# Kernel optimization log

Measured on AMD Instinct MI355X. Metric: run time of the kernel, lower is better.

Reference implementation:

```python
import jax, jax.numpy as jnp
import numpy as np

# dims
B, S, T, F = 8, 1024, 32, 64       # batch, stocks(nodes), seq_len, feature
DWV = 64                            # d_word_vec == d_model
RNN = 64                            # GRU hidden (rnn_unit)
NHID = 128                          # n_hid
NH, DK, DV = 4, 16, 16              # heads, d_k, d_v
NC, NE = 2, 128                     # n_class, num hyperedges (H.shape[1])


def setup_inputs() -> dict:
    key = jax.random.key(0)
    ks = jax.random.split(key, 24)
    def p(i, shape):
        return jax.random.normal(ks[i], shape, jnp.float32) / np.float32(np.sqrt(shape[-1]))
    return {
        'src_seq': jax.random.normal(ks[0], (B, S, T, F), jnp.float32),
        'H': jax.random.normal(ks[1], (S, NE), jnp.float32) * 0.1,
        'adj': jax.random.normal(ks[2], (S, S), jnp.float32) * 0.02,
        'n_hid': NHID,
        # GCN (feature -> n_hid -> feature), shared across both adj and H_new branches
        'gcn_W1': p(3, (F, NHID)), 'gcn_b1': jnp.zeros((NHID,), jnp.float32),
        'gcn_W2': p(4, (NHID, F)), 'gcn_b2': jnp.zeros((F,), jnp.float32),
        # Linear(H.shape[1] -> H.shape[0]) created inside forward
        'Wm': p(5, (S, NE)) * 0.1, 'bm': jnp.zeros((S,), jnp.float32),
        # Linear(feature -> d_word_vec)
        'Wl': p(6, (DWV, F)), 'bl': jnp.zeros((DWV,), jnp.float32),
        # 2-layer GRU (batch_first), torch layout W_{ir|iz|in} stacked
        'Wx0': p(7, (3 * RNN, DWV)), 'Wh0': p(8, (3 * RNN, RNN)),
        'bx0': jnp.zeros((3 * RNN,), jnp.float32), 'bh0': jnp.zeros((3 * RNN,), jnp.float32),
        'Wx1': p(9, (3 * RNN, RNN)), 'Wh1': p(10, (3 * RNN, RNN)),
        'bx1': jnp.zeros((3 * RNN,), jnp.float32), 'bh1': jnp.zeros((3 * RNN,), jnp.float32),
        # temporal multi-head attention
        'Wq': p(11, (NH * DK, RNN)), 'Wk': p(12, (NH * DK, RNN)), 'Wv': p(13, (NH * DV, RNN)),
        'Wo': p(14, (RNN, NH * DV)),
        'ln_g': jnp.ones((RNN,), jnp.float32), 'ln_b': jnp.zeros((RNN,), jnp.float32),
        # HGN: two graph-conv layers over stocks, (T*RNN -> n_hid -> n_hid)
        'Wg1': p(15, (T * RNN, NHID)), 'Wg2': p(16, (NHID, NHID)),
        # tgt_word_prj: n_hid -> n_class (no bias)
        'Wp': p(17, (NC, NHID)),
    }


def reference(src_seq, H, adj, n_hid, gcn_W1, gcn_b1, gcn_W2, gcn_b2, Wm, bm,
              Wl, bl, Wx0, Wh0, bx0, bh0, Wx1, Wh1, bx1, bh1,
              Wq, Wk, Wv, Wo, ln_g, ln_b, Wg1, Wg2, Wp):
    b, s, t, f = src_seq.shape

    # per-timestep GCN over the stock (node) axis, fully batched (replaces the
    # double Python loop of mm+spmm in the original)
    def gcn(x, A):  # x: (b,s,t,f), A: (s,s)
        h = jax.nn.relu(jnp.einsum('nm,bmth->bnth', A, x @ gcn_W1) + gcn_b1)
        return jnp.einsum('nm,bmtf->bntf', A, h @ gcn_W2) + gcn_b2

    H_new = H @ Wm.T + bm                       # (s,s) learned hypergraph adjacency
    z = gcn(src_seq, adj) + gcn(src_seq, H_new)  # y_i + y_f for all timesteps

    x = (z @ Wl.T + bl).reshape(b * s, t, -1)    # (N, T, DWV)
    n = b * s

    def gru_layer(xin, Wx, Wh, bx, bh):
        hdim = Wh.shape[1]
        xp = xin @ Wx.T + bx                      # precompute input projections (N,T,3H)
        def step(h, xt):
            gh = h @ Wh.T + bh
            xr, xz, xn = jnp.split(xt, 3, -1)
            hr, hz, hn = jnp.split(gh, 3, -1)
            r = jax.nn.sigmoid(xr + hr)
            zg = jax.nn.sigmoid(xz + hz)
            cand = jnp.tanh(xn + r * hn)
            hnew = (1.0 - zg) * cand + zg * h
            return hnew, hnew
        h0 = jnp.zeros((xin.shape[0], hdim), xin.dtype)
        _, ys = jax.lax.scan(step, h0, jnp.swapaxes(xp, 0, 1))
        return jnp.swapaxes(ys, 0, 1)

    r = gru_layer(gru_layer(x, Wx0, Wh0, bx0, bh0), Wx1, Wh1, bx1, bh1)  # (N,T,RNN)

    # temporal multi-head self-attention with causal (subsequent) mask
    q = (r @ Wq.T).reshape(n, t, NH, DK)
    k = (r @ Wk.T).reshape(n, t, NH, DK)
    v = (r @ Wv.T).reshape(n, t, NH, DV)
    scores = jnp.einsum('nqhd,nkhd->nhqk', q, k) / np.float32(np.sqrt(DK))
    causal = jnp.triu(jnp.ones((t, t), bool), 1)
    attn = jax.nn.softmax(jnp.where(causal, jnp.float32(-1e9), scores), -1)
    o = jnp.einsum('nhqk,nkhd->nqhd', attn, v).reshape(n, t, NH * DV) @ Wo.T + r
    mu = o.mean(-1, keepdims=True)
    o = (o - mu) / jnp.sqrt(o.var(-1, keepdims=True) + 1e-6) * ln_g + ln_b

    enc = o.reshape(b, s, t * o.shape[-1])        # (b, s, T*RNN)

    # HGN: two graph convolutions over the stock axis -> (b, s, n_hid)
    hg = jax.nn.relu(jnp.einsum('nm,bmd->bnd', adj, enc @ Wg1))
    hg = jnp.einsum('nm,bmd->bnd', adj, hg @ Wg2)

    return hg.reshape(b * s, -1) @ Wp.T           # x_logit_scale = 1.0 (no weight sharing)
```

## Files before the change

kernel.cpp:

```cpp
#include <hip/hip_runtime.h>

typedef __attribute__((ext_vector_type(8))) short bf8;
typedef __attribute__((ext_vector_type(4))) float f4;

__device__ __forceinline__ ushort f2b(float f) {
  union { float f; unsigned u; } v; v.f = f;
  unsigned u = v.u + 0x7FFFu + ((v.u >> 16) & 1u);
  return (ushort)(u >> 16);
}
__device__ __forceinline__ float b2f(ushort h) {
  union { unsigned u; float f; } v; v.u = ((unsigned)h) << 16; return v.f;
}
__device__ __forceinline__ bf8 pack8(const float* p) {
  f4 a = *(const f4*)p; f4 b = *(const f4*)(p + 4);
  bf8 t;
  t[0] = (short)f2b(a[0]); t[1] = (short)f2b(a[1]);
  t[2] = (short)f2b(a[2]); t[3] = (short)f2b(a[3]);
  t[4] = (short)f2b(b[0]); t[5] = (short)f2b(b[1]);
  t[6] = (short)f2b(b[2]); t[7] = (short)f2b(b[3]);
  return t;
}
__device__ __forceinline__ float sigm(float x) { return 1.f / (1.f + __expf(-x)); }
__device__ __forceinline__ float tanh_f(float x) {
  float a = fabsf(x), e = __expf(-2.f * a);
  return copysignf((1.f - e) / (1.f + e), x);
}

__device__ __forceinline__ void gl16(const void* g, void* l) {
  __builtin_amdgcn_global_load_lds(
      (const __attribute__((address_space(1))) unsigned int*)(uintptr_t)g,
      (__attribute__((address_space(3))) unsigned int*)(uintptr_t)l, 16, 0, 0);
}

#define SFENCE __builtin_amdgcn_sched_barrier(0)
#define RAWBAR { __builtin_amdgcn_s_barrier(); SFENCE; }
#define WAIT_LGKM0 { asm volatile("s_waitcnt lgkmcnt(0)" ::: "memory"); SFENCE; }
#define WAIT_VM(n) { asm volatile("s_waitcnt vmcnt(" #n ")" ::: "memory"); SFENCE; }

__global__ __launch_bounds__(256) void cvt_k(const float* __restrict__ in,
                                             ushort* __restrict__ out, int n4) {
  int i = blockIdx.x * 256 + threadIdx.x;
  if (i < n4) {
    f4 v = ((const f4*)in)[i];
    ushort4 o;
    o.x = f2b(v[0]); o.y = f2b(v[1]); o.z = f2b(v[2]); o.w = f2b(v[3]);
    ((ushort4*)out)[i] = o;
  }
}

__global__ __launch_bounds__(256) void cvtT_k(const float* __restrict__ in,
                                              ushort* __restrict__ out, int R, int C) {
  __shared__ ushort t[64][68];
  const int tid = threadIdx.x;
  const int r0 = blockIdx.x * 64, c0 = blockIdx.y * 64;
  #pragma unroll
  for (int it = 0; it < 4; ++it) {
    int r = (tid >> 4) + 16 * it, c = (tid & 15) * 4;
    f4 v = *(const f4*)(in + (long)(r0 + r) * C + c0 + c);
    #pragma unroll
    for (int j = 0; j < 4; ++j) t[c + j][r] = f2b(v[j]);
  }
  __syncthreads();
  #pragma unroll
  for (int it = 0; it < 4; ++it) {
    int cc = (tid >> 4) + 16 * it, rr = (tid & 15) * 4;
    ushort4 o = { t[cc][rr], t[cc][rr + 1], t[cc][rr + 2], t[cc][rr + 3] };
    *(ushort4*)(out + (long)(c0 + cc) * R + r0 + rr) = o;
  }
}

__global__ __launch_bounds__(256) void cat_k(const ushort* __restrict__ a,
                                             const ushort* __restrict__ h,
                                             ushort* __restrict__ o) {
  int i = blockIdx.x * 256 + threadIdx.x;
  int s = i >> 7, c8 = (i & 127) << 3;
  *(int4*)(o + (long)s * 2048 + c8) = *(const int4*)(a + (long)s * 1024 + c8);
  *(int4*)(o + (long)s * 2048 + 1024 + c8) = *(const int4*)(h + (long)s * 1024 + c8);
}

__global__ void wcombT_k(const float* __restrict__ Wl, const float* __restrict__ W2,
                         ushort* __restrict__ out) {
  int idx = blockIdx.x * 256 + threadIdx.x;
  int d = idx >> 7, h = idx & 127;
  float s = 0.f;
  #pragma unroll
  for (int f = 0; f < 64; ++f) s += Wl[d * 64 + f] * W2[h * 64 + f];
  out[d * 128 + h] = f2b(s);
}
__global__ void biasc_k(const float* __restrict__ gb2, const float* __restrict__ Wl,
                        const float* __restrict__ bl, float* __restrict__ bc) {
  int d = threadIdx.x;
  float s = 0.f;
  #pragma unroll
  for (int f = 0; f < 64; ++f) s += gb2[f] * Wl[d * 64 + f];
  bc[d] = 2.f * s + bl[d];
}
__global__ void wfin_k(const float* __restrict__ Wg2, const float* __restrict__ Wp,
                       float* __restrict__ wf) {
  int idx = threadIdx.x;
  int d = idx >> 1, c = idx & 1;
  float s = 0.f;
  #pragma unroll
  for (int e = 0; e < 128; ++e) s += Wg2[d * 128 + e] * Wp[c * 128 + e];
  wf[idx] = s;
}

template<int BIASMODE, int RELU, int OUTMODE>
__global__ __launch_bounds__(512, 2) void gemm3_k(
    const ushort* __restrict__ A, const ushort* __restrict__ B,
    ushort* __restrict__ C, const float* __restrict__ bias, int biasMask,
    int N, int K, int lda, int ldb, int ldc,
    long sAq, long sBq, long sCq)
{
  __shared__ __align__(16) ushort As[2 * 256 * 64];
  __shared__ __align__(16) ushort Bs[2 * 256 * 64];
  const int tid = threadIdx.x, lane = tid & 63, wv = tid >> 6;
  const int wm = wv >> 2, wn = wv & 3;
  const long bm = (long)blockIdx.x * 256, bn = (long)blockIdx.y * 256;
  const int z = blockIdx.z;
  const ushort* Ap = A + (long)z * sAq + bm * lda;
  const ushort* Bp = B + (long)z * sBq + bn * ldb;
  ushort* Cp = C + (long)z * sCq;
  const int nt = K >> 6;

  const int srow = wv * 32 + (lane >> 3);
  const int scol = ((lane & 7) ^ (srow & 7)) << 3;
  const ushort* apb = Ap + (long)srow * lda + scol;
  const ushort* bpb = Bp + (long)srow * ldb + scol;

  #define STAGE3(T, D) { \
    const ushort* ap_ = apb + (T) * 64; \
    const ushort* bp_ = bpb + (T) * 64; \
    ushort* la_ = &As[(D) * 16384 + (wv * 32) * 64]; \
    ushort* lb_ = &Bs[(D) * 16384 + (wv * 32) * 64]; \
    _Pragma("unroll") \
    for (int i_ = 0; i_ < 4; ++i_) gl16(ap_ + (long)(i_ * 8) * lda, la_ + i_ * 512); \
    _Pragma("unroll") \
    for (int i_ = 0; i_ < 4; ++i_) gl16(bp_ + (long)(i_ * 8) * ldb, lb_ + i_ * 512); \
  }

  STAGE3(0, 0);
  if (nt > 1) { STAGE3(1, 1); WAIT_VM(8); }
  else        { WAIT_VM(0); }
  RAWBAR;

  f4 acc[8][4] = {};
  for (int t = 0; t < nt; ++t) {
    const int d = t & 1;
    const ushort* as = As + d * 16384;
    const ushort* bs = Bs + d * 16384;
    bf8 b0[4], a0[8];
    #pragma unroll
    for (int n = 0; n < 4; ++n) {
      int r = wn * 64 + n * 16 + (lane & 15);
      b0[n] = *(const bf8*)(bs + r * 64 + (((lane >> 4) ^ (r & 7)) << 3));
    }
    #pragma unroll
    for (int m = 0; m < 8; ++m) {
      int r = wm * 128 + m * 16 + (lane & 15);
      a0[m] = *(const bf8*)(as + r * 64 + (((lane >> 4) ^ (r & 7)) << 3));
    }
    __builtin_amdgcn_s_setprio(1);
    #pragma unroll
    for (int m = 0; m < 8; ++m)
      #pragma unroll
      for (int n = 0; n < 4; ++n)
        acc[m][n] = __builtin_amdgcn_mfma_f32_16x16x32_bf16(a0[m], b0[n], acc[m][n], 0, 0, 0);
    __builtin_amdgcn_s_setprio(0);
    bf8 b1[4], a1[8];
    #pragma unroll
    for (int n = 0; n < 4; ++n) {
      int r = wn * 64 + n * 16 + (lane & 15);
      b1[n] = *(const bf8*)(bs + r * 64 + (((4 + (lane >> 4)) ^ (r & 7)) << 3));
    }
    #pragma unroll
    for (int m = 0; m < 8; ++m) {
      int r = wm * 128 + m * 16 + (lane & 15);
      a1[m] = *(const bf8*)(as + r * 64 + (((4 + (lane >> 4)) ^ (r & 7)) << 3));
    }
    WAIT_LGKM0;
    RAWBAR;
    if (t + 2 < nt) STAGE3(t + 2, d);
    __builtin_amdgcn_s_setprio(1);
    #pragma unroll
    for (int m = 0; m < 8; ++m)
      #pragma unroll
      for (int n = 0; n < 4; ++n)
        acc[m][n] = __builtin_amdgcn_mfma_f32_16x16x32_bf16(a1[m], b1[n], acc[m][n], 0, 0, 0);
    __builtin_amdgcn_s_setprio(0);
    if (t + 1 < nt) {
      if (t + 2 < nt) { WAIT_VM(8); }
      else            { WAIT_VM(0); }
      RAWBAR;
    }
  }
  #undef STAGE3

  #pragma unroll
  for (int m = 0; m < 8; ++m) {
    int grow = (int)bm + wm * 128 + m * 16 + ((lane >> 4) << 2);
    #pragma unroll
    for (int n = 0; n < 4; ++n) {
      int col = (int)bn + wn * 64 + n * 16 + (lane & 15);
      if (OUTMODE == 2) {
        int hh = grow & 127, tt = grow >> 7;
        ushort4 o;
        o.x = f2b(acc[m][n][0]); o.y = f2b(acc[m][n][1]);
        o.z = f2b(acc[m][n][2]); o.w = f2b(acc[m][n][3]);
        *(ushort4*)(Cp + ((long)col * 32 + tt) * 128 + hh) = o;
      } else {
        #pragma unroll
        for (int rr = 0; rr < 4; ++rr) {
          float v = acc[m][n][rr];
          if (BIASMODE == 1) v += bias[col & biasMask];
          if (BIASMODE == 2) v += bias[(grow + rr) & biasMask];
          if (RELU) v = fmaxf(v, 0.f);
          Cp[(long)(grow + rr) * ldc + col] = f2b(v);
        }
      }
    }
  }
}

template<int BIASMODE, int RELU, int OUTMODE, int SWZ>
__global__ __launch_bounds__(256) void gemm2_k(
    const ushort* __restrict__ A, const ushort* __restrict__ B,
    ushort* __restrict__ C, const float* __restrict__ bias, int biasMask,
    int N, int K, int lda, int ldb, int ldc, int ZD,
    long sAq, long sAr, long sBq, long sBr, long sCq, long sCr)
{
  __shared__ __align__(16) ushort As[2 * 128 * 64];
  __shared__ __align__(16) ushort Bs[2 * 128 * 64];
  const int tid = threadIdx.x, lane = tid & 63, wv = tid >> 6;
  const int wm = wv >> 1, wn = wv & 1;
  int bx = blockIdx.x, by = blockIdx.y;
  if (SWZ) {
    int f = bx + by * gridDim.x;
    int q = f >> 3;
    by = q % gridDim.y;
    bx = (f & 7) + 8 * (q / gridDim.y);
  }
  const long bm = (long)bx * 128, bn = (long)by * 128;
  int z = blockIdx.z, zq = z, zr = 0;
  if (ZD > 1) { zq = z / ZD; zr = z - zq * ZD; }
  const ushort* Ap = A + (long)zq * sAq + (long)zr * sAr + bm * lda;
  const ushort* Bp = B + (long)zq * sBq + (long)zr * sBr + bn * ldb;
  ushort* Cp = C + (long)zq * sCq + (long)zr * sCr;
  const int nt = K >> 6;

  const int srow = wv * 32 + (lane >> 3);
  const int scol = ((lane & 7) ^ (srow & 7)) << 3;
  const ushort* apb = Ap + (long)srow * lda + scol;
  const ushort* bpb = Bp + (long)srow * ldb + scol;

  #define STAGE(T, D) { \
    const ushort* ap_ = apb + (T) * 64; \
    const ushort* bp_ = bpb + (T) * 64; \
    ushort* la_ = &As[((D) * 128 + wv * 32) * 64]; \
    ushort* lb_ = &Bs[((D) * 128 + wv * 32) * 64]; \
    _Pragma("unroll") \
    for (int i_ = 0; i_ < 4; ++i_) gl16(ap_ + (long)(i_ * 8) * lda, la_ + i_ * 512); \
    _Pragma("unroll") \
    for (int i_ = 0; i_ < 4; ++i_) gl16(bp_ + (long)(i_ * 8) * ldb, lb_ + i_ * 512); \
  }

  STAGE(0, 0);
  if (nt > 1) { STAGE(1, 1); WAIT_VM(8); }
  else        { WAIT_VM(0); }
  RAWBAR;

  f4 acc[4][4] = {};
  for (int t = 0; t < nt; ++t) {
    const int d = t & 1;
    const ushort* as = As + d * 8192;
    const ushort* bs = Bs + d * 8192;
    bf8 af[4][2], bfv[4][2];
    #pragma unroll
    for (int mi = 0; mi < 4; ++mi) {
      int r = wm * 64 + mi * 16 + (lane & 15);
      #pragma unroll
      for (int kk = 0; kk < 2; ++kk) {
        int blk = kk * 4 + (lane >> 4);
        af[mi][kk] = *(const bf8*)(as + r * 64 + ((blk ^ (r & 7)) << 3));
      }
    }
    #pragma unroll
    for (int ni = 0; ni < 4; ++ni) {
      int r = wn * 64 + ni * 16 + (lane & 15);
      #pragma unroll
      for (int kk = 0; kk < 2; ++kk) {
        int blk = kk * 4 + (lane >> 4);
        bfv[ni][kk] = *(const bf8*)(bs + r * 64 + ((blk ^ (r & 7)) << 3));
      }
    }
    WAIT_LGKM0;
    RAWBAR;
    if (t + 2 < nt) STAGE(t + 2, d);
    #pragma unroll
    for (int kk = 0; kk < 2; ++kk)
      #pragma unroll
      for (int mi = 0; mi < 4; ++mi)
        #pragma unroll
        for (int ni = 0; ni < 4; ++ni)
          acc[mi][ni] = __builtin_amdgcn_mfma_f32_16x16x32_bf16(af[mi][kk], bfv[ni][kk], acc[mi][ni], 0, 0, 0);
    if (t + 1 < nt) {
      if (t + 2 < nt) { WAIT_VM(8); }
      else            { WAIT_VM(0); }
      RAWBAR;
    }
  }
  #undef STAGE

  #pragma unroll
  for (int mi = 0; mi < 4; ++mi)
    #pragma unroll
    for (int ni = 0; ni < 4; ++ni) {
      int col = (int)bn + wn * 64 + ni * 16 + (lane & 15);
      if (col < N) {
        if (OUTMODE == 2) {
          int hh = wm * 64 + mi * 16 + (lane >> 4) * 4;
          int tt = (int)(bm >> 7);
          ushort4 o;
          o.x = f2b(acc[mi][ni][0]); o.y = f2b(acc[mi][ni][1]);
          o.z = f2b(acc[mi][ni][2]); o.w = f2b(acc[mi][ni][3]);
          *(ushort4*)(Cp + ((long)col * 32 + tt) * 128 + hh) = o;
        } else {
          #pragma unroll
          for (int rr = 0; rr < 4; ++rr) {
            int row = (int)bm + wm * 64 + mi * 16 + (lane >> 4) * 4 + rr;
            float v = acc[mi][ni][rr];
            if (BIASMODE == 1) v += bias[col & biasMask];
            if (BIASMODE == 2) v += bias[row & biasMask];
            if (RELU) v = fmaxf(v, 0.f);
            Cp[(long)row * ldc + col] = f2b(v);
          }
        }
      }
    }
}

template<int BIASMODE, int RELU, int FULLB, int OUTMODE, int SWZ>
__global__ __launch_bounds__(256) void gemm_k(
    const ushort* __restrict__ A, const ushort* __restrict__ B,
    ushort* __restrict__ C, const float* __restrict__ bias, int biasMask,
    int N, int K, int lda, int ldb, int ldc, int ZD,
    long sAq, long sAr, long sBq, long sBr, long sCq, long sCr)
{
  __shared__ __align__(16) ushort As[128 * 64];
  __shared__ __align__(16) ushort Bs[128 * 64];
  const int tid = threadIdx.x, lane = tid & 63, wv = tid >> 6;
  const int wm = wv >> 1, wn = wv & 1;
  int bx = blockIdx.x, by = blockIdx.y;
  const long bm = (long)bx * 128, bn = (long)by * 128;
  int z = blockIdx.z, zq = z, zr = 0;
  if (ZD > 1) { zq = z / ZD; zr = z - zq * ZD; }
  const ushort* Ap = A + (long)zq * sAq + (long)zr * sAr + bm * lda;
  const ushort* Bp = B + (long)zq * sBq + (long)zr * sBr + bn * ldb;
  ushort* Cp = C + (long)zq * sCq + (long)zr * sCr;
  f4 acc[4][4] = {};
  for (int k0 = 0; k0 < K; k0 += 64) {
    #pragma unroll
    for (int i = 0; i < 4; ++i) {
      int row = wv * 32 + i * 8 + (lane >> 3);
      int gc = k0 + (((lane & 7) ^ (row & 7)) << 3);
      gl16(Ap + (long)row * lda + gc, &As[(wv * 32 + i * 8) * 64]);
    }
    if (FULLB) {
      #pragma unroll
      for (int i = 0; i < 4; ++i) {
        int row = wv * 32 + i * 8 + (lane >> 3);
        int gc = k0 + (((lane & 7) ^ (row & 7)) << 3);
        gl16(Bp + (long)row * ldb + gc, &Bs[(wv * 32 + i * 8) * 64]);
      }
    } else {
      #pragma unroll
      for (int i = 0; i < 4; ++i) {
        int row = (tid >> 3) + 32 * i;
        int b8 = tid & 7;
        int4 v = {0, 0, 0, 0};
        if (bn + row < N) v = *(const int4*)(Bp + (long)row * ldb + k0 + ((b8 ^ (row & 7)) << 3));
        *(int4*)(&Bs[row * 64 + b8 * 8]) = v;
      }
    }
    __syncthreads();
    bf8 af[4][2], bfv[4][2];
    #pragma unroll
    for (int mi = 0; mi < 4; ++mi) {
      int r = wm * 64 + mi * 16 + (lane & 15);
      #pragma unroll
      for (int kk = 0; kk < 2; ++kk) {
        int blk = kk * 4 + (lane >> 4);
        af[mi][kk] = *(const bf8*)(&As[r * 64 + ((blk ^ (r & 7)) << 3)]);
      }
    }
    #pragma unroll
    for (int ni = 0; ni < 4; ++ni) {
      int r = wn * 64 + ni * 16 + (lane & 15);
      #pragma unroll
      for (int kk = 0; kk < 2; ++kk) {
        int blk = kk * 4 + (lane >> 4);
        bfv[ni][kk] = *(const bf8*)(&Bs[r * 64 + ((blk ^ (r & 7)) << 3)]);
      }
    }
    #pragma unroll
    for (int kk = 0; kk < 2; ++kk)
      #pragma unroll
      for (int mi = 0; mi < 4; ++mi)
        #pragma unroll
        for (int ni = 0; ni < 4; ++ni)
          acc[mi][ni] = __builtin_amdgcn_mfma_f32_16x16x32_bf16(af[mi][kk], bfv[ni][kk], acc[mi][ni], 0, 0, 0);
    __syncthreads();
  }
  #pragma unroll
  for (int mi = 0; mi < 4; ++mi)
    #pragma unroll
    for (int ni = 0; ni < 4; ++ni) {
      int col = (int)bn + wn * 64 + ni * 16 + (lane & 15);
      if (col < N) {
        #pragma unroll
        for (int rr = 0; rr < 4; ++rr) {
          int row = (int)bm + wm * 64 + mi * 16 + (lane >> 4) * 4 + rr;
          float v = acc[mi][ni][rr];
          if (BIASMODE == 1) v += bias[col & biasMask];
          if (BIASMODE == 2) v += bias[row & biasMask];
          if (RELU) v = fmaxf(v, 0.f);
          long oidx;
          if (OUTMODE == 1) oidx = ((long)(row & 31) * 8192 + (row >> 5)) * 64 + col;
          else              oidx = (long)row * ldc + col;
          Cp[oidx] = f2b(v);
        }
      }
    }
}

__global__ __launch_bounds__(256, 2) void gru_k(
    const ushort* __restrict__ xT,
    const float* __restrict__ Wx0, const float* __restrict__ Wh0,
    const float* __restrict__ bx0, const float* __restrict__ bh0,
    const float* __restrict__ Wx1, const float* __restrict__ Wh1,
    const float* __restrict__ bx1, const float* __restrict__ bh1,
    ushort* __restrict__ rout)
{
  __shared__ ushort hbf[2][2][1024];
  const int tid = threadIdx.x, lane = tid & 63, w = tid >> 6;
  const int seq0 = blockIdx.x * 16;
  for (int i = tid; i < 4096; i += 256) ((ushort*)hbf)[i] = 0;

  const float* Wxp[2] = {Wx0, Wx1};
  const float* Whp[2] = {Wh0, Wh1};
  const float* bxp[2] = {bx0, bx1};
  const float* bhp[2] = {bh0, bh1};
  bf8 Wxf[2][3][2], Whf[2][3][2];
  float bxv[2][3], bhv[2][3];
  #pragma unroll
  for (int L = 0; L < 2; ++L)
    #pragma unroll
    for (int g = 0; g < 3; ++g) {
      int row = g * 64 + w * 16 + (lane & 15);
      bxv[L][g] = bxp[L][row];
      bhv[L][g] = bhp[L][row];
      #pragma unroll
      for (int kk = 0; kk < 2; ++kk) {
        int kb = kk * 32 + (lane >> 4) * 8;
        Wxf[L][g][kk] = pack8(Wxp[L] + row * 64 + kb);
        Whf[L][g][kk] = pack8(Whp[L] + row * 64 + kb);
      }
    }
  __syncthreads();

  const int arow = lane & 15;
  const int col = w * 16 + (lane & 15);
  f4 hprev[2] = {{0.f,0.f,0.f,0.f},{0.f,0.f,0.f,0.f}};
  int pv = 0;
  for (int t = 0; t < 32; ++t) {
    const int cur = pv ^ 1;
    #pragma unroll
    for (int L = 0; L < 2; ++L) {
      bf8 axf[2], ahf[2];
      if (L == 0) {
        const ushort* xb = xT + ((long)t * 8192 + seq0 + arow) * 64 + (lane >> 4) * 8;
        axf[0] = *(const bf8*)(xb);
        axf[1] = *(const bf8*)(xb + 32);
      } else {
        #pragma unroll
        for (int kk = 0; kk < 2; ++kk) {
          int blk = kk * 4 + (lane >> 4);
          axf[kk] = *(const bf8*)(&hbf[0][cur][arow * 64 + ((blk ^ (arow & 7)) << 3)]);
        }
      }
      #pragma unroll
      for (int kk = 0; kk < 2; ++kk) {
        int blk = kk * 4 + (lane >> 4);
        ahf[kk] = *(const bf8*)(&hbf[L][pv][arow * 64 + ((blk ^ (arow & 7)) << 3)]);
      }
      f4 aX[3] = {}; f4 aH[3] = {};
      #pragma unroll
      for (int kk = 0; kk < 2; ++kk)
        #pragma unroll
        for (int g = 0; g < 3; ++g) {
          aX[g] = __builtin_amdgcn_mfma_f32_16x16x32_bf16(axf[kk], Wxf[L][g][kk], aX[g], 0, 0, 0);
          aH[g] = __builtin_amdgcn_mfma_f32_16x16x32_bf16(ahf[kk], Whf[L][g][kk], aH[g], 0, 0, 0);
        }
      f4 hn;
      #pragma unroll
      for (int r = 0; r < 4; ++r) {
        float rg = sigm(aX[0][r] + bxv[L][0] + aH[0][r] + bhv[L][0]);
        float zg = sigm(aX[1][r] + bxv[L][1] + aH[1][r] + bhv[L][1]);
        float cand = tanh_f(aX[2][r] + bxv[L][2] + rg * (aH[2][r] + bhv[L][2]));
        hn[r] = (1.f - zg) * cand + zg * hprev[L][r];
      }
      hprev[L] = hn;
      #pragma unroll
      for (int r = 0; r < 4; ++r) {
        int row = (lane >> 4) * 4 + r;
        ushort hb = f2b(hn[r]);
        hbf[L][cur][row * 64 + (((col >> 3) ^ (row & 7)) << 3) + (col & 7)] = hb;
        if (L == 1) rout[((long)(seq0 + row) * 32 + t) * 64 + col] = hb;
      }
      __syncthreads();
    }
    pv = cur;
  }
}

__global__ __launch_bounds__(256) void attn_k(
    const ushort* __restrict__ r,
    const float* __restrict__ Wq, const float* __restrict__ Wk,
    const float* __restrict__ Wv, const float* __restrict__ Wo,
    const float* __restrict__ lng, const float* __restrict__ lnb,
    ushort* __restrict__ enc)
{
  __shared__ ushort q_s[4][32][40];
  __shared__ ushort k_s[4][32][40];
  __shared__ ushort v_s[4][16][40];
  __shared__ ushort p_s[4][32][40];
  __shared__ ushort o_s[32][88];
  __shared__ float  ln_s[32][68];
  const int tid = threadIdx.x, lane = tid & 63, w = tid >> 6;
  const long n = blockIdx.x;

  for (int i = tid; i < 4 * 32 * 40; i += 256) { ((ushort*)q_s)[i] = 0; ((ushort*)k_s)[i] = 0; }

  bf8 wqf[2], wkf[2], wvf[2], wof[2];
  #pragma unroll
  for (int kk = 0; kk < 2; ++kk) {
    int row = w * 16 + (lane & 15);
    int kb = kk * 32 + (lane >> 4) * 8;
    wqf[kk] = pack8(Wq + row * 64 + kb);
    wkf[kk] = pack8(Wk + row * 64 + kb);
    wvf[kk] = pack8(Wv + row * 64 + kb);
    wof[kk] = pack8(Wo + row * 64 + kb);
  }
  __syncthreads();

  bf8 ar[2][2];
  #pragma unroll
  for (int mi = 0; mi < 2; ++mi)
    #pragma unroll
    for (int kk = 0; kk < 2; ++kk)
      ar[mi][kk] = *(const bf8*)(r + (n * 32 + mi * 16 + (lane & 15)) * 64 + kk * 32 + (lane >> 4) * 8);
  f4 aq[2] = {}, ak[2] = {}, av[2] = {};
  #pragma unroll
  for (int kk = 0; kk < 2; ++kk)
    #pragma unroll
    for (int mi = 0; mi < 2; ++mi) {
      aq[mi] = __builtin_amdgcn_mfma_f32_16x16x32_bf16(ar[mi][kk], wqf[kk], aq[mi], 0, 0, 0);
      ak[mi] = __builtin_amdgcn_mfma_f32_16x16x32_bf16(ar[mi][kk], wkf[kk], ak[mi], 0, 0, 0);
      av[mi] = __builtin_amdgcn_mfma_f32_16x16x32_bf16(ar[mi][kk], wvf[kk], av[mi], 0, 0, 0);
    }
  #pragma unroll
  for (int mi = 0; mi < 2; ++mi)
    #pragma unroll
    for (int rr = 0; rr < 4; ++rr) {
      int row = mi * 16 + (lane >> 4) * 4 + rr;
      q_s[w][row][lane & 15] = f2b(aq[mi][rr]);
      k_s[w][row][lane & 15] = f2b(ak[mi][rr]);
      v_s[w][lane & 15][row] = f2b(av[mi][rr]);
    }

  bf8 a_q[2], b_k[2];
  #pragma unroll
  for (int mt = 0; mt < 2; ++mt)
    a_q[mt] = *(const bf8*)(&q_s[w][mt * 16 + (lane & 15)][(lane >> 4) * 8]);
  #pragma unroll
  for (int nt = 0; nt < 2; ++nt)
    b_k[nt] = *(const bf8*)(&k_s[w][nt * 16 + (lane & 15)][(lane >> 4) * 8]);
  f4 s_[2][2] = {};
  #pragma unroll
  for (int mt = 0; mt < 2; ++mt)
    #pragma unroll
    for (int nt = 0; nt < 2; ++nt)
      s_[mt][nt] = __builtin_amdgcn_mfma_f32_16x16x32_bf16(a_q[mt], b_k[nt], s_[mt][nt], 0, 0, 0);
  #pragma unroll
  for (int mt = 0; mt < 2; ++mt)
    #pragma unroll
    for (int rr = 0; rr < 4; ++rr) {
      int trow = mt * 16 + (lane >> 4) * 4 + rr;
      float s0 = s_[mt][0][rr] * 0.25f, s1 = s_[mt][1][rr] * 0.25f;
      int c0 = lane & 15, c1 = 16 + (lane & 15);
      if (c0 > trow) s0 = -1e30f;
      if (c1 > trow) s1 = -1e30f;
      float m = fmaxf(s0, s1);
      #pragma unroll
      for (int d = 1; d < 16; d <<= 1) m = fmaxf(m, __shfl_xor(m, d));
      float e0 = __expf(s0 - m), e1 = __expf(s1 - m);
      float sum = e0 + e1;
      #pragma unroll
      for (int d = 1; d < 16; d <<= 1) sum += __shfl_xor(sum, d);
      float inv = 1.f / sum;
      p_s[w][trow][c0] = f2b(e0 * inv);
      p_s[w][trow][c1] = f2b(e1 * inv);
    }

  bf8 b_v = *(const bf8*)(&v_s[w][lane & 15][(lane >> 4) * 8]);
  f4 o_[2] = {};
  #pragma unroll
  for (int mt = 0; mt < 2; ++mt) {
    bf8 a_p = *(const bf8*)(&p_s[w][mt * 16 + (lane & 15)][(lane >> 4) * 8]);
    o_[mt] = __builtin_amdgcn_mfma_f32_16x16x32_bf16(a_p, b_v, o_[mt], 0, 0, 0);
  }
  #pragma unroll
  for (int mt = 0; mt < 2; ++mt)
    #pragma unroll
    for (int rr = 0; rr < 4; ++rr)
      o_s[mt * 16 + (lane >> 4) * 4 + rr][w * 16 + (lane & 15)] = f2b(o_[mt][rr]);
  __syncthreads();

  bf8 a_o[2][2];
  #pragma unroll
  for (int mt = 0; mt < 2; ++mt)
    #pragma unroll
    for (int kk = 0; kk < 2; ++kk)
      a_o[mt][kk] = *(const bf8*)(&o_s[mt * 16 + (lane & 15)][kk * 32 + (lane >> 4) * 8]);
  f4 oo[2] = {};
  #pragma unroll
  for (int kk = 0; kk < 2; ++kk)
    #pragma unroll
    for (int mt = 0; mt < 2; ++mt)
      oo[mt] = __builtin_amdgcn_mfma_f32_16x16x32_bf16(a_o[mt][kk], wof[kk], oo[mt], 0, 0, 0);
  #pragma unroll
  for (int mt = 0; mt < 2; ++mt)
    #pragma unroll
    for (int rr = 0; rr < 4; ++rr) {
      int row = mt * 16 + (lane >> 4) * 4 + rr;
      int col = w * 16 + (lane & 15);
      float resid = b2f(r[(n * 32 + row) * 64 + col]);
      ln_s[row][col] = oo[mt][rr] + resid;
    }
  __syncthreads();

  {
    int row = tid >> 3, seg = tid & 7;
    float vals[8], sm = 0.f, sq = 0.f;
    #pragma unroll
    for (int j = 0; j < 8; ++j) {
      float v = ln_s[row][seg * 8 + j];
      vals[j] = v; sm += v; sq += v * v;
    }
    #pragma unroll
    for (int d = 1; d < 8; d <<= 1) { sm += __shfl_xor(sm, d); sq += __shfl_xor(sq, d); }
    float mu = sm * (1.f / 64.f);
    float var = sq * (1.f / 64.f) - mu * mu;
    float rs = rsqrtf(var + 1e-6f);
    union { ushort u[8]; int4 v; } ou;
    #pragma unroll
    for (int j = 0; j < 8; ++j) {
      int c = seg * 8 + j;
      ou.u[j] = f2b((vals[j] - mu) * rs * lng[c] + lnb[c]);
    }
    *(int4*)(enc + (n * 32 + row) * 64 + seg * 8) = ou.v;
  }
}

__global__ __launch_bounds__(256) void final2_k(const ushort* __restrict__ hg3aT,
                                                const float* __restrict__ wf,
                                                float* __restrict__ out) {
  int i = blockIdx.x * 256 + threadIdx.x;
  int b = i >> 10, s = i & 1023;
  const ushort* base = hg3aT + (long)b * 131072 + s;
  float a0 = 0.f, a1 = 0.f;
  #pragma unroll
  for (int d = 0; d < 128; ++d) {
    float v = b2f(base[d * 1024]);
    a0 += v * wf[2 * d];
    a1 += v * wf[2 * d + 1];
  }
  out[2 * i] = a0; out[2 * i + 1] = a1;
}

extern "C" void kernel_launch(void* const* d_in, const int* in_sizes, int n_in,
                              void* d_out, int out_size, void* d_ws, size_t ws_size,
                              hipStream_t stream) {
  const float* src = (const float*)d_in[0];
  const float* H   = (const float*)d_in[1];
  const float* adj = (const float*)d_in[2];
  const float* gW1 = (const float*)d_in[4];
  const float* gb1 = (const float*)d_in[5];
  const float* gW2 = (const float*)d_in[6];
  const float* gb2 = (const float*)d_in[7];
  const float* Wm  = (const float*)d_in[8];
  const float* bm  = (const float*)d_in[9];
  const float* Wl  = (const float*)d_in[10];
  const float* bl  = (const float*)d_in[11];
  const float* Wx0 = (const float*)d_in[12];
  const float* Wh0 = (const float*)d_in[13];
  const float* bx0 = (const float*)d_in[14];
  const float* bh0 = (const float*)d_in[15];
  const float* Wx1 = (const float*)d_in[16];
  const float* Wh1 = (const float*)d_in[17];
  const float* bx1 = (const float*)d_in[18];
  const float* bh1 = (const float*)d_in[19];
  const float* Wq  = (const float*)d_in[20];
  const float* Wk  = (const float*)d_in[21];
  const float* Wv  = (const float*)d_in[22];
  const float* Wo  = (const float*)d_in[23];
  const float* lng = (const float*)d_in[24];
  const float* lnb = (const float*)d_in[25];
  const float* Wg1 = (const float*)d_in[26];
  const float* Wg2 = (const float*)d_in[27];
  const float* Wp  = (const float*)d_in[28];

  char* ws = (char*)d_ws;
  const size_t MB = 1048576ull;
  ushort* adj_bf  = (ushort*)(ws);
  ushort* Hnew_bf = (ushort*)(ws + 2 * MB);
  ushort* H_bf    = (ushort*)(ws + 4 * MB);
  ushort* Wm_bf   = (ushort*)(ws + 4 * MB + 262144);
  ushort* W1T     = (ushort*)(ws + 4 * MB + 524288);
  ushort* WcT     = (ushort*)(ws + 4 * MB + 524288 + 16384);
  float*  bc      = (float*) (ws + 4 * MB + 524288 + 32768);
  float*  wfin    = (float*) (ws + 4 * MB + 524288 + 33792);
  ushort* Wg1T    = (ushort*)(ws + 5 * MB);
  ushort* src_bf  = (ushort*)(ws + 6 * MB);
  ushort* adjcat  = (ushort*)(ws + 6 * MB);
  ushort* XT      = (ushort*)(ws + 38 * MB);
  ushort* Psum    = (ushort*)(ws + 38 * MB);
  ushort* h1cat   = (ushort*)(ws + 102 * MB);
  ushort* enc     = (ushort*)(ws + 102 * MB);
  ushort* g1T     = (ushort*)(ws + 134 * MB);
  ushort* hgT     = (ushort*)(ws + 136 * MB);
  ushort* hg3aT   = (ushort*)(ws + 138 * MB);
  ushort* xT      = (ushort*)(ws + 166 * MB);
  ushort* r_bf    = (ushort*)(ws + 198 * MB);

  auto CVT = [&](const float* in, ushort* out, int n) {
    int n4 = n >> 2;
    cvt_k<<<dim3((n4 + 255) / 256), dim3(256), 0, stream>>>(in, out, n4);
  };
  CVT(src, src_bf, 16777216);
  CVT(adj, adj_bf, 1048576);
  CVT(H, H_bf, 131072);
  CVT(Wm, Wm_bf, 131072);
  cvtT_k<<<dim3(1, 2), 256, 0, stream>>>(gW1, W1T, 64, 128);
  cvtT_k<<<dim3(32, 2), 256, 0, stream>>>(Wg1, Wg1T, 2048, 128);
  wcombT_k<<<dim3(32), 256, 0, stream>>>(Wl, gW2, WcT);
  biasc_k<<<dim3(1), 64, 0, stream>>>(gb2, Wl, bl, bc);
  wfin_k<<<dim3(1), 256, 0, stream>>>(Wg2, Wp, wfin);

  gemm2_k<1,0,0,0><<<dim3(8,8,1),256,0,stream>>>(H_bf, Wm_bf, Hnew_bf, bm, 1023,
      1024, 128, 128, 128, 1024, 1, 0,0, 0,0, 0,0);
  gemm2_k<0,0,0,0><<<dim3(1,8,256),256,0,stream>>>(W1T, src_bf, XT, nullptr, 0,
      1024, 64, 64, 2048, 1024, 32, 0,0, 2097152,64, 4194304,131072);
  cat_k<<<dim3(512),256,0,stream>>>(adj_bf, Hnew_bf, adjcat);
  gemm3_k<2,1,0><<<dim3(16,8,8),512,0,stream>>>(XT, adj_bf, h1cat, gb1, 127,
      2048, 1024, 1024, 1024, 2048, 4194304, 0, 8388608);
  gemm3_k<0,0,2><<<dim3(16,4,8),512,0,stream>>>(h1cat, adjcat, Psum, nullptr, 0,
      1024, 2048, 2048, 2048, 0, 8388608, 0, 4194304);
  gemm_k<1,0,0,1,0><<<dim3(2048,1,1),256,0,stream>>>(Psum, WcT, xT, bc, 63,
      64, 128, 128, 128, 64, 1, 0,0, 0,0, 0,0);
  gru_k<<<dim3(512),dim3(256),0,stream>>>(xT, Wx0,Wh0,bx0,bh0, Wx1,Wh1,bx1,bh1, r_bf);
  attn_k<<<dim3(8192),dim3(256),0,stream>>>(r_bf, Wq,Wk,Wv,Wo, lng,lnb, enc);
  gemm2_k<0,0,0,0><<<dim3(1,8,8),256,0,stream>>>(Wg1T, enc, g1T, nullptr, 0,
      1024, 2048, 2048, 2048, 1024, 1, 0,0, 2097152,0, 131072,0);
  gemm2_k<0,1,0,0><<<dim3(1,8,8),256,0,stream>>>(g1T, adj_bf, hgT, nullptr, 0,
      1024, 1024, 1024, 1024, 1024, 1, 131072,0, 0,0, 131072,0);
  gemm2_k<0,0,0,0><<<dim3(1,8,8),256,0,stream>>>(hgT, adj_bf, hg3aT, nullptr, 0,
      1024, 1024, 1024, 1024, 1024, 1, 131072,0, 0,0, 131072,0);
  final2_k<<<dim3(32),256,0,stream>>>(hg3aT, wfin, (float*)d_out);
}
```

Baseline: 617.6 us.

## Split-K the three tail HGN GEMMs and unroll gemm3 double-buffer loop

The three small tail GEMMs (Wg1 projection and two adjacency convolutions) launched only 64 blocks each, which leaves most CUs idle. They now use a 4-way split-K kernel writing fp32 partials, followed by a reduction kernel that sums the partials and applies ReLU and the bf16 conversion. This quadruples the block count at the cost of extra fp32 partial traffic and three more launches. Separately, the gemm3 main loop is unrolled by two with precomputed LDS base pointers to cut address arithmetic, and the unused SWZ remap in gemm2 is removed.

```diff
diff --git a/kernel.cpp b/kernel.cpp
--- a/kernel.cpp
+++ b/kernel.cpp
@@ -139,59 +139,80 @@
     for (int i_ = 0; i_ < 4; ++i_) gl16(bp_ + (long)(i_ * 8) * ldb, lb_ + i_ * 512); \
   }
 
+  const int lr = lane & 15, lq = lane >> 4, l7 = lane & 7;
+  const ushort* aB0 = As + (wm * 128 + lr) * 64 + ((lq ^ l7) << 3);
+  const ushort* aB1 = As + (wm * 128 + lr) * 64 + (((4 + lq) ^ l7) << 3);
+  const ushort* bB0 = Bs + (wn * 64 + lr) * 64 + ((lq ^ l7) << 3);
+  const ushort* bB1 = Bs + (wn * 64 + lr) * 64 + (((4 + lq) ^ l7) << 3);
+
   STAGE3(0, 0);
   if (nt > 1) { STAGE3(1, 1); WAIT_VM(8); }
   else        { WAIT_VM(0); }
   RAWBAR;
 
   f4 acc[8][4] = {};
-  for (int t = 0; t < nt; ++t) {
-    const int d = t & 1;
-    const ushort* as = As + d * 16384;
-    const ushort* bs = Bs + d * 16384;
-    bf8 b0[4], a0[8];
-    #pragma unroll
-    for (int n = 0; n < 4; ++n) {
-      int r = wn * 64 + n * 16 + (lane & 15);
-      b0[n] = *(const bf8*)(bs + r * 64 + (((lane >> 4) ^ (r & 7)) << 3));
-    }
-    #pragma unroll
-    for (int m = 0; m < 8; ++m) {
-      int r = wm * 128 + m * 16 + (lane & 15);
-      a0[m] = *(const bf8*)(as + r * 64 + (((lane >> 4) ^ (r & 7)) << 3));
-    }
-    __builtin_amdgcn_s_setprio(1);
-    #pragma unroll
-    for (int m = 0; m < 8; ++m)
-      #pragma unroll
-      for (int n = 0; n < 4; ++n)
-        acc[m][n] = __builtin_amdgcn_mfma_f32_16x16x32_bf16(a0[m], b0[n], acc[m][n], 0, 0, 0);
-    __builtin_amdgcn_s_setprio(0);
-    bf8 b1[4], a1[8];
-    #pragma unroll
-    for (int n = 0; n < 4; ++n) {
-      int r = wn * 64 + n * 16 + (lane & 15);
-      b1[n] = *(const bf8*)(bs + r * 64 + (((4 + (lane >> 4)) ^ (r & 7)) << 3));
-    }
-    #pragma unroll
-    for (int m = 0; m < 8; ++m) {
-      int r = wm * 128 + m * 16 + (lane & 15);
-      a1[m] = *(const bf8*)(as + r * 64 + (((4 + (lane >> 4)) ^ (r & 7)) << 3));
-    }
-    WAIT_LGKM0;
-    RAWBAR;
-    if (t + 2 < nt) STAGE3(t + 2, d);
-    __builtin_amdgcn_s_setprio(1);
-    #pragma unroll
-    for (int m = 0; m < 8; ++m)
-      #pragma unroll
-      for (int n = 0; n < 4; ++n)
-        acc[m][n] = __builtin_amdgcn_mfma_f32_16x16x32_bf16(a1[m], b1[n], acc[m][n], 0, 0, 0);
-    __builtin_amdgcn_s_setprio(0);
-    if (t + 1 < nt) {
+  for (int t = 0; t < nt; t += 2) {
+    {
+      bf8 b0[4], a0[8];
+      #pragma unroll
+      for (int n = 0; n < 4; ++n) b0[n] = *(const bf8*)(bB0 + n * 1024);
+      #pragma unroll
+      for (int m = 0; m < 8; ++m) a0[m] = *(const bf8*)(aB0 + m * 1024);
+      __builtin_amdgcn_s_setprio(1);
+      #pragma unroll
+      for (int m = 0; m < 8; ++m)
+        #pragma unroll
+        for (int n = 0; n < 4; ++n)
+          acc[m][n] = __builtin_amdgcn_mfma_f32_16x16x32_bf16(a0[m], b0[n], acc[m][n], 0, 0, 0);
+      __builtin_amdgcn_s_setprio(0);
+      bf8 b1[4], a1[8];
+      #pragma unroll
+      for (int n = 0; n < 4; ++n) b1[n] = *(const bf8*)(bB1 + n * 1024);
+      #pragma unroll
+      for (int m = 0; m < 8; ++m) a1[m] = *(const bf8*)(aB1 + m * 1024);
+      WAIT_LGKM0;
+      RAWBAR;
+      if (t + 2 < nt) STAGE3(t + 2, 0);
+      __builtin_amdgcn_s_setprio(1);
+      #pragma unroll
+      for (int m = 0; m < 8; ++m)
+        #pragma unroll
+        for (int n = 0; n < 4; ++n)
+          acc[m][n] = __builtin_amdgcn_mfma_f32_16x16x32_bf16(a1[m], b1[n], acc[m][n], 0, 0, 0);
+      __builtin_amdgcn_s_setprio(0);
       if (t + 2 < nt) { WAIT_VM(8); }
       else            { WAIT_VM(0); }
       RAWBAR;
+    }
+    {
+      bf8 b0[4], a0[8];
+      #pragma unroll
+      for (int n = 0; n < 4; ++n) b0[n] = *(const bf8*)(bB0 + 16384 + n * 1024);
+      #pragma unroll
+      for (int m = 0; m < 8; ++m) a0[m] = *(const bf8*)(aB0 + 16384 + m * 1024);
+      __builtin_amdgcn_s_setprio(1);
+      #pragma unroll
+      for (int m = 0; m < 8; ++m)
+        #pragma unroll
+        for (int n = 0; n < 4; ++n)
+          acc[m][n] = __builtin_amdgcn_mfma_f32_16x16x32_bf16(a0[m], b0[n], acc[m][n], 0, 0, 0);
+      __builtin_amdgcn_s_setprio(0);
+      bf8 b1[4], a1[8];
+      #pragma unroll
+      for (int n = 0; n < 4; ++n) b1[n] = *(const bf8*)(bB1 + 16384 + n * 1024);
+      #pragma unroll
+      for (int m = 0; m < 8; ++m) a1[m] = *(const bf8*)(aB1 + 16384 + m * 1024);
+      WAIT_LGKM0;
+      RAWBAR;
+      if (t + 2 < nt) STAGE3(t + 3, 1);
+      __builtin_amdgcn_s_setprio(1);
+      #pragma unroll
+      for (int m = 0; m < 8; ++m)
+        #pragma unroll
+        for (int n = 0; n < 4; ++n)
+          acc[m][n] = __builtin_amdgcn_mfma_f32_16x16x32_bf16(a1[m], b1[n], acc[m][n], 0, 0, 0);
+      __builtin_amdgcn_s_setprio(0);
+      if (t + 2 < nt) { WAIT_VM(8); RAWBAR; }
     }
   }
   #undef STAGE3
@@ -234,12 +255,6 @@
   const int tid = threadIdx.x, lane = tid & 63, wv = tid >> 6;
   const int wm = wv >> 1, wn = wv & 1;
   int bx = blockIdx.x, by = blockIdx.y;
-  if (SWZ) {
-    int f = bx + by * gridDim.x;
-    int q = f >> 3;
-    by = q % gridDim.y;
-    bx = (f & 7) + 8 * (q / gridDim.y);
-  }
   const long bm = (long)bx * 128, bn = (long)by * 128;
   int z = blockIdx.z, zq = z, zr = 0;
   if (ZD > 1) { zq = z / ZD; zr = z - zq * ZD; }
@@ -337,6 +352,118 @@
         }
       }
     }
+}
+
+__global__ __launch_bounds__(256) void gemmsk_k(
+    const ushort* __restrict__ A, const ushort* __restrict__ B,
+    float* __restrict__ P, int Kc, int lda, int ldb,
+    long sAq, long sBq)
+{
+  __shared__ __align__(16) ushort As[2 * 128 * 64];
+  __shared__ __align__(16) ushort Bs[2 * 128 * 64];
+  const int tid = threadIdx.x, lane = tid & 63, wv = tid >> 6;
+  const int wm = wv >> 1, wn = wv & 1;
+  const long bm = (long)blockIdx.x * 128, bn = (long)blockIdx.y * 128;
+  const int kc = blockIdx.z & 3, zq = blockIdx.z >> 2;
+  const ushort* Ap = A + (long)zq * sAq + kc * Kc + bm * lda;
+  const ushort* Bp = B + (long)zq * sBq + kc * Kc + bn * ldb;
+  const int nt = Kc >> 6;
+
+  const int srow = wv * 32 + (lane >> 3);
+  const int scol = ((lane & 7) ^ (srow & 7)) << 3;
+  const ushort* apb = Ap + (long)srow * lda + scol;
+  const ushort* bpb = Bp + (long)srow * ldb + scol;
+
+  #define STAGEK(T, D) { \
+    const ushort* ap_ = apb + (T) * 64; \
+    const ushort* bp_ = bpb + (T) * 64; \
+    ushort* la_ = &As[((D) * 128 + wv * 32) * 64]; \
+    ushort* lb_ = &Bs[((D) * 128 + wv * 32) * 64]; \
+    _Pragma("unroll") \
+    for (int i_ = 0; i_ < 4; ++i_) gl16(ap_ + (long)(i_ * 8) * lda, la_ + i_ * 512); \
+    _Pragma("unroll") \
+    for (int i_ = 0; i_ < 4; ++i_) gl16(bp_ + (long)(i_ * 8) * ldb, lb_ + i_ * 512); \
+  }
+
+  STAGEK(0, 0);
+  if (nt > 1) { STAGEK(1, 1); WAIT_VM(8); }
+  else        { WAIT_VM(0); }
+  RAWBAR;
+
+  f4 acc[4][4] = {};
+  for (int t = 0; t < nt; ++t) {
+    const int d = t & 1;
+    const ushort* as = As + d * 8192;
+    const ushort* bs = Bs + d * 8192;
+    bf8 af[4][2], bfv[4][2];
+    #pragma unroll
+    for (int mi = 0; mi < 4; ++mi) {
+      int r = wm * 64 + mi * 16 + (lane & 15);
+      #pragma unroll
+      for (int kk = 0; kk < 2; ++kk) {
+        int blk = kk * 4 + (lane >> 4);
+        af[mi][kk] = *(const bf8*)(as + r * 64 + ((blk ^ (r & 7)) << 3));
+      }
+    }
+    #pragma unroll
+    for (int ni = 0; ni < 4; ++ni) {
+      int r = wn * 64 + ni * 16 + (lane & 15);
+      #pragma unroll
+      for (int kk = 0; kk < 2; ++kk) {
+        int blk = kk * 4 + (lane >> 4);
+        bfv[ni][kk] = *(const bf8*)(bs + r * 64 + ((blk ^ (r & 7)) << 3));
+      }
+    }
+    WAIT_LGKM0;
+    RAWBAR;
+    if (t + 2 < nt) STAGEK(t + 2, d);
+    #pragma unroll
+    for (int kk = 0; kk < 2; ++kk)
+      #pragma unroll
+      for (int mi = 0; mi < 4; ++mi)
+        #pragma unroll
+        for (int ni = 0; ni < 4; ++ni)
+          acc[mi][ni] = __builtin_amdgcn_mfma_f32_16x16x32_bf16(af[mi][kk], bfv[ni][kk], acc[mi][ni], 0, 0, 0);
+    if (t + 1 < nt) {
+      if (t + 2 < nt) { WAIT_VM(8); }
+      else            { WAIT_VM(0); }
+      RAWBAR;
+    }
+  }
+  #undef STAGEK
+
+  float* Pp = P + (long)blockIdx.z * 131072;
+  #pragma unroll
+  for (int mi = 0; mi < 4; ++mi)
+    #pragma unroll
+    for (int ni = 0; ni < 4; ++ni) {
+      int col = (int)bn + wn * 64 + ni * 16 + (lane & 15);
+      #pragma unroll
+      for (int rr = 0; rr < 4; ++rr) {
+        int row = (int)bm + wm * 64 + mi * 16 + (lane >> 4) * 4 + rr;
+        Pp[(long)row * 1024 + col] = acc[mi][ni][rr];
+      }
+    }
+}
+
+template<int RELU>
+__global__ __launch_bounds__(256) void redk_k(const float* __restrict__ P,
+                                              ushort* __restrict__ C) {
+  int idx = blockIdx.x * 256 + threadIdx.x;
+  long z = idx >> 15;
+  long rem = (long)(idx & 32767) * 4;
+  const float* base = P + z * 4 * 131072 + rem;
+  f4 s = *(const f4*)base;
+  #pragma unroll
+  for (int kc = 1; kc < 4; ++kc) s += *(const f4*)(base + kc * 131072);
+  ushort4 o;
+  #pragma unroll
+  for (int j = 0; j < 4; ++j) {
+    float v = s[j];
+    if (RELU) v = fmaxf(v, 0.f);
+    ((ushort*)&o)[j] = f2b(v);
+  }
+  *(ushort4*)(C + z * 131072 + rem) = o;
 }
 
 template<int BIASMODE, int RELU, int FULLB, int OUTMODE, int SWZ>
@@ -735,6 +862,7 @@
   ushort* adjcat  = (ushort*)(ws + 6 * MB);
   ushort* XT      = (ushort*)(ws + 38 * MB);
   ushort* Psum    = (ushort*)(ws + 38 * MB);
+  float*  Pk      = (float*) (ws + 38 * MB);
   ushort* h1cat   = (ushort*)(ws + 102 * MB);
   ushort* enc     = (ushort*)(ws + 102 * MB);
   ushort* g1T     = (ushort*)(ws + 134 * MB);
@@ -770,11 +898,11 @@
       64, 128, 128, 128, 64, 1, 0,0, 0,0, 0,0);
   gru_k<<<dim3(512),dim3(256),0,stream>>>(xT, Wx0,Wh0,bx0,bh0, Wx1,Wh1,bx1,bh1, r_bf);
   attn_k<<<dim3(8192),dim3(256),0,stream>>>(r_bf, Wq,Wk,Wv,Wo, lng,lnb, enc);
-  gemm2_k<0,0,0,0><<<dim3(1,8,8),256,0,stream>>>(Wg1T, enc, g1T, nullptr, 0,
-      1024, 2048, 2048, 2048, 1024, 1, 0,0, 2097152,0, 131072,0);
-  gemm2_k<0,1,0,0><<<dim3(1,8,8),256,0,stream>>>(g1T, adj_bf, hgT, nullptr, 0,
-      1024, 1024, 1024, 1024, 1024, 1, 131072,0, 0,0, 131072,0);
-  gemm2_k<0,0,0,0><<<dim3(1,8,8),256,0,stream>>>(hgT, adj_bf, hg3aT, nullptr, 0,
-      1024, 1024, 1024, 1024, 1024, 1, 131072,0, 0,0, 131072,0);
+  gemmsk_k<<<dim3(1,8,32),256,0,stream>>>(Wg1T, enc, Pk, 512, 2048, 2048, 0, 2097152);
+  redk_k<0><<<dim3(1024),256,0,stream>>>(Pk, g1T);
+  gemmsk_k<<<dim3(1,8,32),256,0,stream>>>(g1T, adj_bf, Pk, 256, 1024, 1024, 131072, 0);
+  redk_k<1><<<dim3(1024),256,0,stream>>>(Pk, hgT);
+  gemmsk_k<<<dim3(1,8,32),256,0,stream>>>(hgT, adj_bf, Pk, 256, 1024, 1024, 131072, 0);
+  redk_k<0><<<dim3(1024),256,0,stream>>>(Pk, hg3aT);
   final2_k<<<dim3(32),256,0,stream>>>(hg3aT, wfin, (float*)d_out);
 }
```

Result: slower. 1.026 ms (+66.1%).
